# Kernel optimization log

Measured on AMD Instinct MI355X. Metric: run time of the kernel, lower is better.

## Reference

```python
import jax, jax.numpy as jnp
import numpy as np

N = 40000      # nodes
E = 640000     # edges (before self loops)
D = 128        # node_input_dim == hidden_dim
H = 4          # heads
C = 32         # out channels per head (hidden_dim // heads)
G = 512        # number of graphs
NEG_SLOPE = 0.2
BN_EPS = 1e-5
L = 3          # layers


def setup_inputs() -> dict:
    key = jax.random.key(0)
    ks = jax.random.split(key, 20)
    s = 0.1  # weight scale to keep activations sane
    inp = {
        "x": jax.random.normal(ks[0], (N, D), jnp.float32),
        "edge_index": jax.random.randint(ks[1], (2, E), 0, N, jnp.int32),
        "batch": jnp.sort(jax.random.randint(ks[2], (N,), 0, G, jnp.int32)),
        # stacked per-layer GATv2 params (all layers have in=out=128)
        "Wl": jax.random.normal(ks[3], (L, D, H * C), jnp.float32) * s,
        "bl": jax.random.normal(ks[4], (L, H * C), jnp.float32) * s,
        "Wr": jax.random.normal(ks[5], (L, D, H * C), jnp.float32) * s,
        "br": jax.random.normal(ks[6], (L, H * C), jnp.float32) * s,
        "att": jax.random.normal(ks[7], (L, H, C), jnp.float32) * s,
        "conv_bias": jax.random.normal(ks[8], (L, H * C), jnp.float32) * s,
        # BatchNorm (inference mode: running stats)
        "bn_gamma": jnp.ones((L, H * C), jnp.float32),
        "bn_beta": jnp.zeros((L, H * C), jnp.float32),
        "bn_mean": jax.random.normal(ks[9], (L, H * C), jnp.float32) * 0.01,
        "bn_var": jnp.ones((L, H * C), jnp.float32),
        # classifier MLP 128 -> 64 -> 2
        "W1": jax.random.normal(ks[10], (H * C, 64), jnp.float32) * s,
        "b1": jnp.zeros((64,), jnp.float32),
        "W2": jax.random.normal(ks[11], (64, 2), jnp.float32) * s,
        "b2": jnp.zeros((2,), jnp.float32),
    }
    return inp


def _gatv2_layer(x, src, dst, Wl, bl, Wr, br, att, conv_bias):
    # GATv2Conv: e_ij = att . leaky_relu(lin_l(x_j) + lin_r(x_i)); out_i = sum_j softmax_i(e_ij) lin_l(x_j)
    xl = (x @ Wl + bl).reshape(N, H, C)  # source-side transform
    xr = (x @ Wr + br).reshape(N, H, C)  # target-side transform
    e = jax.nn.leaky_relu(xl[src] + xr[dst], NEG_SLOPE)         # [Efull, H, C]
    logits = jnp.einsum("ehc,hc->eh", e, att)                   # [Efull, H]
    m = jax.ops.segment_max(logits, dst, num_segments=N)         # segment softmax over dst
    a = jnp.exp(logits - m[dst])
    denom = jax.ops.segment_sum(a, dst, num_segments=N)
    alpha = a / denom[dst]                                       # self loops guarantee nonempty segments
    out = jax.ops.segment_sum(alpha[:, :, None] * xl[src], dst, num_segments=N)
    return out.reshape(N, H * C) + conv_bias


def reference(x, edge_index, batch, Wl, bl, Wr, br, att, conv_bias,
              bn_gamma, bn_beta, bn_mean, bn_var, W1, b1, W2, b2):
    # add self loops once
    loops = jnp.arange(N, dtype=edge_index.dtype)
    src = jnp.concatenate([edge_index[0], loops])
    dst = jnp.concatenate([edge_index[1], loops])
    h = x
    for i in range(L):
        h = _gatv2_layer(h, src, dst, Wl[i], bl[i], Wr[i], br[i], att[i], conv_bias[i])
        h = (h - bn_mean[i]) * jax.lax.rsqrt(bn_var[i] + BN_EPS) * bn_gamma[i] + bn_beta[i]
        h = jax.nn.relu(h)  # dropout disabled (eval mode)
    # global mean pool per graph
    sums = jax.ops.segment_sum(h, batch, num_segments=G)
    cnts = jax.ops.segment_sum(jnp.ones((N,), h.dtype), batch, num_segments=G)
    pooled = sums / jnp.maximum(cnts, 1.0)[:, None]
    hid = jax.nn.relu(pooled @ W1 + b1)
    return hid @ W2 + b2  # [G, num_classes]
```

## Files before the change

### kernel.cpp

```cpp
#include <hip/hip_runtime.h>
#include <math.h>

typedef unsigned short u16;
typedef unsigned int   u32;
typedef __attribute__((ext_vector_type(8))) short bf16x8;
typedef __attribute__((ext_vector_type(4))) float f32x4;

#define NNODES 40000
#define NEDGES 640000
#define NGRAPH 512
#define EFULL  (NEDGES + NNODES)
#define NB_SCAN ((NNODES + 255) / 256)

__device__ __forceinline__ float bflo(u32 u) {
  union { u32 i; float f; } v; v.i = u << 16; return v.f;
}
__device__ __forceinline__ float bfhi(u32 u) {
  union { u32 i; float f; } v; v.i = u & 0xffff0000u; return v.f;
}
__device__ __forceinline__ u16 f2bf(float f) {
  union { float f; u32 i; } v; v.f = f;
  u32 r = v.i + 0x7fffu + ((v.i >> 16) & 1u);
  return (u16)(r >> 16);
}
__device__ __forceinline__ void unpack8(uint4 u, float* f) {
  f[0] = bflo(u.x); f[1] = bfhi(u.x);
  f[2] = bflo(u.y); f[3] = bfhi(u.y);
  f[4] = bflo(u.z); f[5] = bfhi(u.z);
  f[6] = bflo(u.w); f[7] = bfhi(u.w);
}

__global__ __launch_bounds__(256) void cast_w(const float* __restrict__ Wl, const float* __restrict__ Wr,
                                              u16* __restrict__ Wt) {
  int i = blockIdx.x * 256 + threadIdx.x;
  int k = i & 127, n = (i >> 7) & 127, h = (i >> 14) & 1, L = i >> 15;
  const float* W = h ? Wr : Wl;
  Wt[i] = f2bf(W[(size_t)L * 16384 + k * 128 + n]);
}


__global__ __launch_bounds__(256) void deg_kernel(const int* __restrict__ ei, int* __restrict__ deg) {
  int e = blockIdx.x * 256 + threadIdx.x;
  if (e >= EFULL) return;
  int d = (e < NEDGES) ? ei[NEDGES + e] : (e - NEDGES);
  atomicAdd(&deg[d], 1);
}

__global__ __launch_bounds__(256) void scan_partial(const int* __restrict__ deg,
                                                    int* __restrict__ rowptr, int* __restrict__ btot) {
  __shared__ int s[256];
  int b = blockIdx.x, t = threadIdx.x, i = b * 256 + t;
  int v = (i < NNODES) ? deg[i] : 0;
  s[t] = v;
  __syncthreads();
  for (int st = 1; st < 256; st <<= 1) {
    int u = (t >= st) ? s[t - st] : 0;
    __syncthreads();
    s[t] += u;
    __syncthreads();
  }
  if (i < NNODES) rowptr[i] = s[t] - v;
  if (t == 255) btot[b] = s[255];
}

__global__ __launch_bounds__(256) void scan_btot_k(int* __restrict__ btot) {
  __shared__ int s[256];
  int t = threadIdx.x;
  int v = (t < NB_SCAN) ? btot[t] : 0;
  s[t] = v;
  __syncthreads();
  for (int st = 1; st < 256; st <<= 1) {
    int u = (t >= st) ? s[t - st] : 0;
    __syncthreads();
    s[t] += u;
    __syncthreads();
  }
  if (t < NB_SCAN) btot[t] = s[t] - v;
}

__global__ __launch_bounds__(256) void scan_add(int* __restrict__ rowptr, const int* __restrict__ btot) {
  int b = blockIdx.x, t = threadIdx.x, i = b * 256 + t;
  if (i < NNODES) rowptr[i] += btot[b];
  if (i == 0) rowptr[NNODES] = EFULL;
}

__global__ __launch_bounds__(256) void scatter_kernel(const int* __restrict__ ei, const int* __restrict__ rowptr,
                                                      int* __restrict__ cnt, int* __restrict__ srcs) {
  int e = blockIdx.x * 256 + threadIdx.x;
  if (e >= EFULL) return;
  int s, d;
  if (e < NEDGES) { s = ei[e]; d = ei[NEDGES + e]; } else { s = d = e - NEDGES; }
  int pos = rowptr[d] + atomicAdd(&cnt[d], 1);
  srcs[pos] = s;
}


__global__ __launch_bounds__(256) void gemm_mfma(const u16* __restrict__ A,
                                                 const float* __restrict__ Af32,
                                                 const u16* __restrict__ Wt,
                                                 const float* __restrict__ bl, const float* __restrict__ br,
                                                 u16* __restrict__ xl, u16* __restrict__ xr) {
  __shared__ u16 Ws[128][136];
  int t = threadIdx.x;
  int half = blockIdx.y;
  const u16* Wg = Wt + (size_t)half * 16384;
#pragma unroll
  for (int it = 0; it < 8; ++it) {
    int idx = t * 8 + it * 2048;
    int n = idx >> 7, k = idx & 127;
    *(uint4*)&Ws[n][k] = *(const uint4*)&Wg[idx];
  }
  int lane = t & 63, wave = t >> 6;
  int row0 = blockIdx.x * 64 + wave * 16;
  int m = lane & 15, quad = lane >> 4;
  bf16x8 af[4];
  if (Af32) {
    const float* Ap = Af32 + (size_t)(row0 + m) * 128 + quad * 8;
#pragma unroll
    for (int s = 0; s < 4; ++s) {
      float4 u = *(const float4*)(Ap + s * 32);
      float4 v = *(const float4*)(Ap + s * 32 + 4);
      union { u16 q[8]; bf16x8 b; } pk;
      pk.q[0] = f2bf(u.x); pk.q[1] = f2bf(u.y); pk.q[2] = f2bf(u.z); pk.q[3] = f2bf(u.w);
      pk.q[4] = f2bf(v.x); pk.q[5] = f2bf(v.y); pk.q[6] = f2bf(v.z); pk.q[7] = f2bf(v.w);
      af[s] = pk.b;
    }
  } else {
    const u16* Ap = A + (size_t)(row0 + m) * 128 + quad * 8;
#pragma unroll
    for (int s = 0; s < 4; ++s) af[s] = *(const bf16x8*)(Ap + s * 32);
  }
  __syncthreads();
  const float* bias = half ? br : bl;
  u16* out = half ? xr : xl;
  f32x4 acc[8];
#pragma unroll
  for (int nt = 0; nt < 8; ++nt) acc[nt] = (f32x4){0.f, 0.f, 0.f, 0.f};
#pragma unroll
  for (int nt = 0; nt < 8; ++nt) {
    const u16* wp = &Ws[nt * 16 + m][quad * 8];
#pragma unroll
    for (int s = 0; s < 4; ++s) {
      bf16x8 wf = *(const bf16x8*)(wp + s * 32);
      acc[nt] = __builtin_amdgcn_mfma_f32_16x16x32_bf16(wf, af[s], acc[nt], 0, 0, 0);
    }
  }
  size_t row = row0 + m;
#pragma unroll
  for (int nt = 0; nt < 8; ++nt) {
    int cb = nt * 16 + quad * 4;
    float4 b4 = *(const float4*)(bias + cb);
    u32 lo = (u32)f2bf(acc[nt][0] + b4.x) | ((u32)f2bf(acc[nt][1] + b4.y) << 16);
    u32 hi = (u32)f2bf(acc[nt][2] + b4.z) | ((u32)f2bf(acc[nt][3] + b4.w) << 16);
    uint2 pk; pk.x = lo; pk.y = hi;
    *(uint2*)(out + row * 128 + cb) = pk;
  }
}


__global__ __launch_bounds__(256) void gat_node(const u16* __restrict__ xl, const u16* __restrict__ xr,
    const int* __restrict__ rowptr, const int* __restrict__ srcs,
    const float* __restrict__ att, const float* __restrict__ conv_bias,
    const float* __restrict__ gam, const float* __restrict__ bet,
    const float* __restrict__ bmn, const float* __restrict__ bvr,
    u16* __restrict__ hout) {
  int wave = threadIdx.x >> 6;
  int lane = threadIdx.x & 63;
  int node = blockIdx.x * 4 + wave;
  if (node >= NNODES) return;
  int beg = rowptr[node];
  int end = rowptr[node + 1];
  int lam = lane & 15, grp = lane >> 4;
  int cb = lam * 8;
  float xrv[8], atv[8];
  unpack8(*(const uint4*)(xr + (size_t)node * 128 + cb), xrv);
  {
    float4 a0 = *(const float4*)(att + cb);
    float4 a1 = *(const float4*)(att + cb + 4);
    atv[0] = a0.x; atv[1] = a0.y; atv[2] = a0.z; atv[3] = a0.w;
    atv[4] = a1.x; atv[5] = a1.y; atv[6] = a1.z; atv[7] = a1.w;
  }
  float acc[8] = {0.f, 0.f, 0.f, 0.f, 0.f, 0.f, 0.f, 0.f};
  float den = 0.f;

  for (int base = beg; base < end; base += 64) {
    int lim = end - base; if (lim > 64) lim = 64;
    int sreg = srcs[base + (lane < lim ? lane : 0)];
    int cnt = (lim - grp + 3) >> 2;
    uint4 u_nxt;
    {
      int s0 = __shfl(sreg, grp, 64);
      if (cnt > 0) u_nxt = *(const uint4*)(xl + (size_t)s0 * 128 + cb);
    }
    for (int i = 0; i < cnt; ++i) {
      uint4 u = u_nxt;
      if (i + 1 < cnt) {
        int sn = __shfl(sreg, grp + 4 * (i + 1), 64);
        u_nxt = *(const uint4*)(xl + (size_t)sn * 128 + cb);
      }
      float raw[8];
      unpack8(u, raw);
      float p0 = 0.f, p1 = 0.f;
#pragma unroll
      for (int q = 0; q < 8; ++q) {
        float a = raw[q] + xrv[q];
        float l = fmaxf(a, 0.2f * a);
        if (q & 1) p1 = fmaf(atv[q], l, p1); else p0 = fmaf(atv[q], l, p0);
      }
      float p = p0 + p1;
      p += __shfl_xor(p, 1, 64);
      p += __shfl_xor(p, 2, 64);
      float w = __expf(p);
      den += w;
#pragma unroll
      for (int q = 0; q < 8; ++q) acc[q] = fmaf(w, raw[q], acc[q]);
    }
  }
#pragma unroll
  for (int q = 0; q < 8; ++q) {
    acc[q] += __shfl_xor(acc[q], 16, 64);
    acc[q] += __shfl_xor(acc[q], 32, 64);
  }
  den += __shfl_xor(den, 16, 64);
  den += __shfl_xor(den, 32, 64);
  float e0 = (grp & 2) ? ((grp & 1) ? acc[6] : acc[4]) : ((grp & 1) ? acc[2] : acc[0]);
  float e1 = (grp & 2) ? ((grp & 1) ? acc[7] : acc[5]) : ((grp & 1) ? acc[3] : acc[1]);
  int c2 = cb + 2 * grp;
  float inv = 1.f / den;
  float2 cbv = *(const float2*)(conv_bias + c2);
  float2 mnv = *(const float2*)(bmn + c2);
  float2 vrv = *(const float2*)(bvr + c2);
  float2 gmv = *(const float2*)(gam + c2);
  float2 btv = *(const float2*)(bet + c2);
  float o0 = e0 * inv + cbv.x;
  float o1 = e1 * inv + cbv.y;
  o0 = (o0 - mnv.x) * rsqrtf(vrv.x + 1e-5f) * gmv.x + btv.x;
  o1 = (o1 - mnv.y) * rsqrtf(vrv.y + 1e-5f) * gmv.y + btv.y;
  u32 pk = (u32)f2bf(fmaxf(o0, 0.f)) | ((u32)f2bf(fmaxf(o1, 0.f)) << 16);
  *(u32*)(hout + (size_t)node * 128 + c2) = pk;
}


__device__ __forceinline__ int lowb(const int* __restrict__ batch, int val) {
  int lo = 0, hi = NNODES;
  while (lo < hi) {
    int mid = (lo + hi) >> 1;
    if (batch[mid] < val) lo = mid + 1; else hi = mid;
  }
  return lo;
}

__global__ __launch_bounds__(128) void pool_classify(const u16* __restrict__ h, const int* __restrict__ batch,
    const float* __restrict__ W1, const float* __restrict__ b1,
    const float* __restrict__ W2, const float* __restrict__ b2, float* __restrict__ out) {
  __shared__ float red[2][128];
  __shared__ float pm[128];
  __shared__ float hid[64];
  int g = blockIdx.x, t = threadIdx.x;
  int lo = lowb(batch, g);
  int hi = lowb(batch, g + 1);
  int t63 = t & 63, hh = t >> 6;
  float acc0 = 0.f, acc1 = 0.f;
  for (int n = lo + hh; n < hi; n += 2) {
    u32 u = *(const u32*)(h + (size_t)n * 128 + 2 * t63);
    acc0 += bflo(u); acc1 += bfhi(u);
  }
  red[hh][2 * t63] = acc0; red[hh][2 * t63 + 1] = acc1;
  __syncthreads();
  float cnt = fmaxf((float)(hi - lo), 1.f);
  pm[t] = (red[0][t] + red[1][t]) / cnt;
  __syncthreads();
  if (t < 64) {
    float a = b1[t];
    for (int k = 0; k < 128; ++k) a += pm[k] * W1[k * 64 + t];
    hid[t] = fmaxf(a, 0.f);
  }
  __syncthreads();
  if (t < 2) {
    float o = b2[t];
    for (int k = 0; k < 64; ++k) o += hid[k] * W2[k * 2 + t];
    out[g * 2 + t] = o;
  }
}


extern "C" void kernel_launch(void* const* d_in, const int* in_sizes, int n_in,
                              void* d_out, int out_size, void* d_ws, size_t ws_size,
                              hipStream_t stream) {
  const float* x   = (const float*)d_in[0];
  const int*   ei  = (const int*)d_in[1];
  const int*   bat = (const int*)d_in[2];
  const float* Wl  = (const float*)d_in[3];
  const float* bl  = (const float*)d_in[4];
  const float* Wr  = (const float*)d_in[5];
  const float* br  = (const float*)d_in[6];
  const float* att = (const float*)d_in[7];
  const float* cb  = (const float*)d_in[8];
  const float* gam = (const float*)d_in[9];
  const float* bet = (const float*)d_in[10];
  const float* bmn = (const float*)d_in[11];
  const float* bvr = (const float*)d_in[12];
  const float* W1  = (const float*)d_in[13];
  const float* b1  = (const float*)d_in[14];
  const float* W2  = (const float*)d_in[15];
  const float* b2  = (const float*)d_in[16];
  float* out = (float*)d_out;

  const size_t NF = (size_t)NNODES * 128;
  u16* xlb = (u16*)d_ws;
  u16* xrb = xlb + NF;
  u16* hb0 = xrb + NF;
  u16* hb1 = hb0 + NF;
  u16* Wt  = hb1 + NF;
  int* btot   = (int*)(Wt + 3 * 2 * 128 * 128);
  int* deg    = btot + 256;
  int* rowptr = deg + NNODES;
  int* cnt    = rowptr + NNODES + 1;
  int* srcs   = cnt + NNODES;

  hipMemsetAsync(deg, 0, NNODES * sizeof(int), stream);
  hipMemsetAsync(cnt, 0, NNODES * sizeof(int), stream);

  cast_w<<<98304 / 256, 256, 0, stream>>>(Wl, Wr, Wt);

  int eb = (EFULL + 255) / 256;
  deg_kernel<<<eb, 256, 0, stream>>>(ei, deg);
  scan_partial<<<NB_SCAN, 256, 0, stream>>>(deg, rowptr, btot);
  scan_btot_k<<<1, 256, 0, stream>>>(btot);
  scan_add<<<NB_SCAN, 256, 0, stream>>>(rowptr, btot);
  scatter_kernel<<<eb, 256, 0, stream>>>(ei, rowptr, cnt, srcs);

  const u16* hcur = hb0;
  u16* bufs[2] = {hb0, hb1};
  for (int i = 0; i < 3; ++i) {
    u16* hnext = bufs[i & 1];
    gemm_mfma<<<dim3(NNODES / 64, 2), 256, 0, stream>>>(hcur, i == 0 ? x : nullptr,
        Wt + (size_t)i * 2 * 16384, bl + i * 128, br + i * 128, xlb, xrb);
    gat_node<<<NNODES / 4, 256, 0, stream>>>(xlb, xrb, rowptr, srcs,
        att + i * 128, cb + i * 128, gam + i * 128, bet + i * 128,
        bmn + i * 128, bvr + i * 128, hnext);
    hcur = hnext;
  }
  pool_classify<<<NGRAPH, 128, 0, stream>>>(hcur, bat, W1, b1, W2, b2, out);
}
```

Measured before the change: 322.0 us.

## Cut CSR build launches, reuse atomic ranks, stage GEMM output through LDS

The deg zeroing is folded into the weight-cast kernel, which replaces the two memsets. The degree atomic's return value is stored as a per-edge rank, so the scatter no longer needs a second atomic pass over a count array. The btot scan and the add kernel are merged into one kernel in which every block reduces its own prefix. The GEMM epilogue now stages bf16 results in LDS and writes them as coalesced 16-byte rows, at the cost of an extra rank buffer and two more block barriers.

```diff
diff --git a/kernel.cpp b/kernel.cpp
--- a/kernel.cpp
+++ b/kernel.cpp
@@ -31,19 +31,21 @@
 }
 
 __global__ __launch_bounds__(256) void cast_w(const float* __restrict__ Wl, const float* __restrict__ Wr,
-                                              u16* __restrict__ Wt) {
+                                              u16* __restrict__ Wt, int* __restrict__ deg) {
   int i = blockIdx.x * 256 + threadIdx.x;
   int k = i & 127, n = (i >> 7) & 127, h = (i >> 14) & 1, L = i >> 15;
   const float* W = h ? Wr : Wl;
   Wt[i] = f2bf(W[(size_t)L * 16384 + k * 128 + n]);
-}
-
-
-__global__ __launch_bounds__(256) void deg_kernel(const int* __restrict__ ei, int* __restrict__ deg) {
+  if (i < NNODES) deg[i] = 0;
+}
+
+
+__global__ __launch_bounds__(256) void deg_rank(const int* __restrict__ ei, int* __restrict__ deg,
+                                                int* __restrict__ rank) {
   int e = blockIdx.x * 256 + threadIdx.x;
   if (e >= EFULL) return;
   int d = (e < NEDGES) ? ei[NEDGES + e] : (e - NEDGES);
-  atomicAdd(&deg[d], 1);
+  rank[e] = atomicAdd(&deg[d], 1);
 }
 
 __global__ __launch_bounds__(256) void scan_partial(const int* __restrict__ deg,
@@ -63,35 +65,30 @@
   if (t == 255) btot[b] = s[255];
 }
 
-__global__ __launch_bounds__(256) void scan_btot_k(int* __restrict__ btot) {
+__global__ __launch_bounds__(256) void scan_finish(int* __restrict__ rowptr, const int* __restrict__ btot) {
   __shared__ int s[256];
-  int t = threadIdx.x;
-  int v = (t < NB_SCAN) ? btot[t] : 0;
-  s[t] = v;
-  __syncthreads();
-  for (int st = 1; st < 256; st <<= 1) {
-    int u = (t >= st) ? s[t - st] : 0;
+  int b = blockIdx.x, t = threadIdx.x;
+  s[t] = (t < b && t < NB_SCAN) ? btot[t] : 0;
+  __syncthreads();
+  for (int st = 128; st; st >>= 1) {
+    if (t < st) s[t] += s[t + st];
     __syncthreads();
-    s[t] += u;
-    __syncthreads();
-  }
-  if (t < NB_SCAN) btot[t] = s[t] - v;
-}
-
-__global__ __launch_bounds__(256) void scan_add(int* __restrict__ rowptr, const int* __restrict__ btot) {
-  int b = blockIdx.x, t = threadIdx.x, i = b * 256 + t;
-  if (i < NNODES) rowptr[i] += btot[b];
+  }
+  int prefix = s[0];
+  int i = b * 256 + t;
+  if (i < NNODES) rowptr[i] += prefix;
   if (i == 0) rowptr[NNODES] = EFULL;
 }
 
-__global__ __launch_bounds__(256) void scatter_kernel(const int* __restrict__ ei, const int* __restrict__ rowptr,
-                                                      int* __restrict__ cnt, int* __restrict__ srcs) {
+__global__ __launch_bounds__(256) void scatter_kernel(const int* __restrict__ ei,
+                                                      const int* __restrict__ rowptr,
+                                                      const int* __restrict__ rank,
+                                                      int* __restrict__ srcs) {
   int e = blockIdx.x * 256 + threadIdx.x;
   if (e >= EFULL) return;
   int s, d;
   if (e < NEDGES) { s = ei[e]; d = ei[NEDGES + e]; } else { s = d = e - NEDGES; }
-  int pos = rowptr[d] + atomicAdd(&cnt[d], 1);
-  srcs[pos] = s;
+  srcs[rowptr[d] + rank[e]] = s;
 }
 
 
@@ -145,7 +142,9 @@
       acc[nt] = __builtin_amdgcn_mfma_f32_16x16x32_bf16(wf, af[s], acc[nt], 0, 0, 0);
     }
   }
-  size_t row = row0 + m;
+  __syncthreads();
+  u16 (*St)[136] = (u16(*)[136])Ws;
+  int row_l = wave * 16 + m;
 #pragma unroll
   for (int nt = 0; nt < 8; ++nt) {
     int cb = nt * 16 + quad * 4;
@@ -153,8 +152,13 @@
     u32 lo = (u32)f2bf(acc[nt][0] + b4.x) | ((u32)f2bf(acc[nt][1] + b4.y) << 16);
     u32 hi = (u32)f2bf(acc[nt][2] + b4.z) | ((u32)f2bf(acc[nt][3] + b4.w) << 16);
     uint2 pk; pk.x = lo; pk.y = hi;
-    *(uint2*)(out + row * 128 + cb) = pk;
-  }
+    *(uint2*)&St[row_l][cb] = pk;
+  }
+  __syncthreads();
+  int row = t >> 2, cs = (t & 3) * 32;
+  uint4* gp = (uint4*)(out + (size_t)(blockIdx.x * 64 + row) * 128 + cs);
+#pragma unroll
+  for (int k = 0; k < 4; ++k) gp[k] = *(uint4*)&St[row][cs + k * 8];
 }
 
 
@@ -315,20 +319,16 @@
   int* btot   = (int*)(Wt + 3 * 2 * 128 * 128);
   int* deg    = btot + 256;
   int* rowptr = deg + NNODES;
-  int* cnt    = rowptr + NNODES + 1;
-  int* srcs   = cnt + NNODES;
-
-  hipMemsetAsync(deg, 0, NNODES * sizeof(int), stream);
-  hipMemsetAsync(cnt, 0, NNODES * sizeof(int), stream);
-
-  cast_w<<<98304 / 256, 256, 0, stream>>>(Wl, Wr, Wt);
+  int* rank   = rowptr + NNODES + 1;
+  int* srcs   = rank + EFULL;
+
+  cast_w<<<98304 / 256, 256, 0, stream>>>(Wl, Wr, Wt, deg);
 
   int eb = (EFULL + 255) / 256;
-  deg_kernel<<<eb, 256, 0, stream>>>(ei, deg);
+  deg_rank<<<eb, 256, 0, stream>>>(ei, deg, rank);
   scan_partial<<<NB_SCAN, 256, 0, stream>>>(deg, rowptr, btot);
-  scan_btot_k<<<1, 256, 0, stream>>>(btot);
-  scan_add<<<NB_SCAN, 256, 0, stream>>>(rowptr, btot);
-  scatter_kernel<<<eb, 256, 0, stream>>>(ei, rowptr, cnt, srcs);
+  scan_finish<<<NB_SCAN, 256, 0, stream>>>(rowptr, btot);
+  scatter_kernel<<<eb, 256, 0, stream>>>(ei, rowptr, rank, srcs);
 
   const u16* hcur = hb0;
   u16* bufs[2] = {hb0, hb1};
```

Result: faster. 293.5 us (-8.9%).
